# Optimization experiments

Measured on AMD Instinct MI355X. Metric: run time of the kernel, lower is better.

Reference implementation:

```python
import jax, jax.numpy as jnp
import numpy as np

N, C, T, V = 16, 64, 512, 25
R, O, S = 8, 64, 3  # rel_channels, out_channels, num_subset


def setup_inputs() -> dict:
    key = jax.random.key(0)
    ks = jax.random.split(key, 12)
    sc = 0.05
    return {
        "x": jax.random.normal(ks[0], (N, C, T, V), jnp.float32),
        "A": jax.random.normal(ks[1], (S, V, V), jnp.float32) * 0.1,
        "alpha": jax.random.normal(ks[2], (1,), jnp.float32) * 0.1,
        "w1": jax.random.normal(ks[3], (S, R, C), jnp.float32) * sc,
        "b1": jax.random.normal(ks[4], (S, R), jnp.float32) * sc,
        "w2": jax.random.normal(ks[5], (S, R, C), jnp.float32) * sc,
        "b2": jax.random.normal(ks[6], (S, R), jnp.float32) * sc,
        "w3": jax.random.normal(ks[7], (S, O, C), jnp.float32) * sc,
        "b3": jax.random.normal(ks[8], (S, O), jnp.float32) * sc,
        "w4": jax.random.normal(ks[9], (S, O, R), jnp.float32) * sc,
        "b4": jax.random.normal(ks[10], (S, O), jnp.float32) * sc,
        "sparse": 0,
    }


def _mask(w, thr):
    # SparseConv2d: magnitude-threshold the 1x1 conv weights at runtime.
    return jnp.where(jnp.abs(w) > thr, w, jnp.zeros_like(w))


def reference(x, A, alpha, w1, b1, w2, b2, w3, b3, w4, b4, sparse):
    thr = jnp.float32(sparse)

    def conv1x1(w, b, inp):  # w [o,c], b [o], inp [n,c,t,v] -> [n,o,t,v]
        return jnp.einsum('oc,nctv->notv', _mask(w, thr), inp) + b[None, :, None, None]

    y = None
    for i in range(A.shape[0]):
        x1 = conv1x1(w1[i], b1[i], x).mean(-2)          # [n,r,v]
        x2 = conv1x1(w2[i], b2[i], x).mean(-2)          # [n,r,v]
        x3 = conv1x1(w3[i], b3[i], x)                   # [n,o,t,v]
        att = jnp.tanh(x1[..., :, None] - x2[..., None, :])  # [n,r,v,v]
        a = jnp.einsum('or,nruv->nouv', _mask(w4[i], thr), att) + b4[i][None, :, None, None]
        a = a * alpha + A[i][None, None]                # [n,o,v,v]
        z = jnp.einsum('ncuv,nctu->nctv', a, x3)        # node aggregation
        y = z if y is None else y + z
    # in_channels == out_channels -> residual is identity
    return jax.nn.relu(y + x)
```

## Files before the change

kernel.cpp:

```cpp
#include <hip/hip_runtime.h>
#include <cmath>

typedef __bf16 bf16x4v __attribute__((ext_vector_type(4)));
typedef __bf16 bf16x8 __attribute__((ext_vector_type(8)));
typedef float f32x4 __attribute__((ext_vector_type(4)));

namespace {
constexpr int kN = 16, kC = 64, kT = 512, kV = 25, kS = 3, kO = 64;
constexpr int kTV = kT * kV;
constexpr size_t WS_AFRAG = 102400;
constexpr size_t WS_W3F = WS_AFRAG + (size_t)48 * 131072;
}

__device__ __forceinline__ int swzA(int col, int cbyte) {
  return ((col << 7) + cbyte) ^ ((col & 7) << 4);
}
__device__ __forceinline__ int swzB(int c, int t, int ubyte) {
  return 32768 + (c << 9) + (((t << 6) + ubyte) ^ ((((c ^ t) & 7)) << 4));
}

__global__ __launch_bounds__(256) void k1_mean(const float* __restrict__ x,
                                               float* __restrict__ xm) {
  const int bid = blockIdx.x;
  __shared__ float part[250][4];
  const int tid = threadIdx.x;
  const float4* xg4 = (const float4*)(x + (size_t)bid * kTV);
  if (tid < 250) {
    float a0 = 0.f, a1 = 0.f, a2 = 0.f, a3 = 0.f;
    for (int j = tid; j < 3200; j += 250) {
      float4 v = xg4[j];
      a0 += v.x; a1 += v.y; a2 += v.z; a3 += v.w;
    }
    part[tid][0] = a0; part[tid][1] = a1; part[tid][2] = a2; part[tid][3] = a3;
  }
  __syncthreads();
  if (tid < 25) {
    float s = 0.f;
#pragma unroll
    for (int r = 0; r < 4; ++r) {
      int q = ((tid - r + 25) % 25) * 19 % 25;
#pragma unroll
      for (int p = 0; p < 10; ++p) s += part[q + 25 * p][r];
    }
    xm[bid * 25 + tid] = s * (1.f / 512.f);
  }
}

__global__ __launch_bounds__(256) void k2_attn(
    const float* __restrict__ xm, const float* __restrict__ Ag,
    const float* __restrict__ alpha, const float* __restrict__ w1,
    const float* __restrict__ b1, const float* __restrict__ w2,
    const float* __restrict__ b2, const float* __restrict__ w3,
    const float* __restrict__ w4, const float* __restrict__ b4,
    const int* __restrict__ sparse, unsigned char* __restrict__ ws) {
  const float thr = (float)sparse[0];
  const int b = blockIdx.x;
  const int s = b >> 6, n = (b >> 2) & 15, q = b & 3;
  __shared__ float xm_l[1600];
  __shared__ float x1_l[200], x2_l[200];
  __shared__ float att_l[8 * 625];
  __shared__ float attsum_l[200];
  __shared__ float ag_l[625];
  __shared__ float acs_l[25];
  __shared__ float w4_l[512];
  const int tid = threadIdx.x;
  for (int i = tid; i < 1600; i += 256) xm_l[i] = xm[n * 1600 + i];
  for (int i = tid; i < 512; i += 256) {
    float w = w4[s * 512 + i];
    w4_l[i] = (fabsf(w) > thr) ? w : 0.f;
  }
  for (int i = tid; i < 625; i += 256) ag_l[i] = Ag[s * 625 + i];
  __syncthreads();
  for (int i = tid; i < 400; i += 256) {
    int which = i / 200, idx = i % 200, r = idx / 25, u = idx % 25;
    const float* wrow = (which == 0 ? w1 : w2) + (s * 8 + r) * 64;
    float acc = 0.f;
    for (int cc = 0; cc < 64; ++cc) {
      float w = wrow[cc];
      w = (fabsf(w) > thr) ? w : 0.f;
      acc += w * xm_l[cc * 25 + u];
    }
    acc += (which == 0 ? b1 : b2)[s * 8 + r];
    if (which == 0) x1_l[idx] = acc;
    else x2_l[idx] = acc;
  }
  __syncthreads();
  for (int i = tid; i < 8 * 625; i += 256) {
    int r = i / 625, uv = i % 625, u = uv / 25, v = uv % 25;
    att_l[i] = tanhf(x1_l[r * 25 + u] - x2_l[r * 25 + v]);
  }
  __syncthreads();
  if (tid < 200) {
    int r = tid / 25, v = tid % 25;
    float sum = 0.f;
    for (int u = 0; u < 25; ++u) sum += att_l[r * 625 + u * 25 + v];
    attsum_l[tid] = sum;
  } else if (tid < 225) {
    int v = tid - 200;
    float sum = 0.f;
    for (int u = 0; u < 25; ++u) sum += ag_l[u * 25 + v];
    acs_l[v] = sum;
  }
  __syncthreads();
  const float al = alpha[0];
  unsigned char* afrag = ws + WS_AFRAG + (size_t)(s * 16 + n) * 131072;
  for (int slot = q * 2048 + tid; slot < (q + 1) * 2048; slot += 256) {
    int c = slot >> 7, vt = (slot >> 6) & 1, l = slot & 63;
    int v = vt * 16 + (l & 15), g = l >> 4;
    bf16x8 out;
    if (v < 25) {
      float b4v = b4[s * 64 + c];
#pragma unroll
      for (int j = 0; j < 8; ++j) {
        int u = g * 8 + j;
        float val = 0.f;
        if (u < 25) {
          float acc = 0.f;
#pragma unroll
          for (int r = 0; r < 8; ++r) acc += w4_l[c * 8 + r] * att_l[r * 625 + u * 25 + v];
          val = al * (acc + b4v) + ag_l[u * 25 + v];
        } else if (u == 25) {
          float acc = 0.f;
#pragma unroll
          for (int r = 0; r < 8; ++r) acc += w4_l[c * 8 + r] * attsum_l[r * 25 + v];
          val = al * acc + 25.f * al * b4v + acs_l[v];
        }
        out[j] = (__bf16)val;
      }
    } else {
#pragma unroll
      for (int j = 0; j < 8; ++j) out[j] = (__bf16)0.f;
    }
    *(bf16x8*)(afrag + (size_t)slot * 16) = out;
  }
  if (n == 0 && tid < 128) {
    unsigned char* w3f = ws + WS_W3F + (size_t)s * 8192;
    int slot = q * 128 + tid;
    int ot = slot >> 7, ks = (slot >> 6) & 1, l = slot & 63;
    int o = ot * 16 + (l & 15), g = l >> 4;
    bf16x8 out;
#pragma unroll
    for (int j = 0; j < 8; ++j) {
      int cp = ks * 32 + g * 8 + j;
      float w = w3[(s * 64 + o) * 64 + cp];
      out[j] = (__bf16)((fabsf(w) > thr) ? w : 0.f);
    }
    *(bf16x8*)(w3f + slot * 16) = out;
  }
}

__global__ __launch_bounds__(512) void k3_main(const float* __restrict__ x,
                                               const float* __restrict__ b3,
                                               const unsigned char* __restrict__ ws,
                                               float* __restrict__ y) {
  const int n = blockIdx.x;
  const int tb = blockIdx.y;
  extern __shared__ __align__(16) unsigned char smem[];
  const int tid = threadIdx.x;
  const int w = tid >> 6, l = tid & 63, g = l >> 4, l15 = l & 15;
  const float4* xg4 = (const float4*)(x + (size_t)n * kC * kTV);

  for (int idx = tid; idx < 448; idx += 512) {
    int col_i = idx >> 3, gb = idx & 7;
    int t = col_i / 7, u = 25 + col_i % 7;
    f32x4 z = {0.f, 0.f, 0.f, 0.f};
    *(f32x4*)(smem + swzA(t * 32 + u, gb * 16)) = z;
  }
  for (int idx = tid; idx < 1536; idx += 512) {
    int pair = idx / 3, k = idx % 3;
    int c = pair >> 3, t = pair & 7;
    *(unsigned int*)(smem + swzB(c, t, 52 + 4 * k)) = 0u;
  }
  for (int i4 = tid; i4 < 3200; i4 += 512) {
    int c = i4 / 50, r4 = i4 % 50;
    float4 vv = xg4[c * 3200 + tb * 50 + r4];
    float vals[4] = {vv.x, vv.y, vv.z, vv.w};
    int lin = r4 * 4;
#pragma unroll
    for (int k = 0; k < 4; ++k) {
      int t = (lin + k) / 25, u = (lin + k) % 25;
      *(__bf16*)(smem + swzA(t * 32 + u, c * 2)) = (__bf16)vals[k];
    }
  }
  __syncthreads();

  const unsigned char* afrag = ws + WS_AFRAG;
  const unsigned char* w3f = ws + WS_W3F;

  f32x4 zacc[8][2];
#pragma unroll
  for (int cc = 0; cc < 8; ++cc)
#pragma unroll
    for (int vt = 0; vt < 2; ++vt) {
      f32x4 zz = {0.f, 0.f, 0.f, 0.f};
      zacc[cc][vt] = zz;
    }

  for (int s = 0; s < kS; ++s) {
    bf16x8 A1[4][2];
#pragma unroll
    for (int ot = 0; ot < 4; ++ot)
#pragma unroll
      for (int ks = 0; ks < 2; ++ks)
        A1[ot][ks] = *(const bf16x8*)(w3f + s * 8192 + ((ot * 2 + ks) * 64 + l) * 16);
    if (s) __syncthreads();

    f32x4 acc[2][4];
#pragma unroll
    for (int cti = 0; cti < 2; ++cti) {
      int col = w * 32 + cti * 16 + l15;
      bf16x8 xa0 = *(const bf16x8*)(smem + swzA(col, g * 16));
      bf16x8 xa1 = *(const bf16x8*)(smem + swzA(col, 64 + g * 16));
#pragma unroll
      for (int ot = 0; ot < 4; ++ot) {
        f32x4 d = {0.f, 0.f, 0.f, 0.f};
        d = __builtin_amdgcn_mfma_f32_16x16x32_bf16(xa0, A1[ot][0], d, 0, 0, 0);
        d = __builtin_amdgcn_mfma_f32_16x16x32_bf16(xa1, A1[ot][1], d, 0, 0, 0);
        acc[cti][ot] = d;
      }
    }
#pragma unroll
    for (int cti = 0; cti < 2; ++cti) {
      int u0 = cti * 16 + g * 4;
#pragma unroll
      for (int ot = 0; ot < 4; ++ot) {
        int c = ot * 16 + l15;
        if (!cti || g < 2) {
          bf16x4v pk;
          pk[0] = (__bf16)acc[cti][ot][0];
          pk[1] = (__bf16)acc[cti][ot][1];
          pk[2] = (__bf16)acc[cti][ot][2];
          pk[3] = (__bf16)acc[cti][ot][3];
          *(bf16x4v*)(smem + swzB(c, w, 2 * u0)) = pk;
        } else if (g == 2) {
          *(__bf16*)(smem + swzB(c, w, 48)) = (__bf16)acc[cti][ot][0];
        }
      }
    }
    {
      int c = tid >> 3, t = tid & 7;
      *(__bf16*)(smem + swzB(c, t, 50)) = (__bf16)b3[s * 64 + c];
    }
    const unsigned char* af = afrag + (size_t)(s * 16 + n) * 131072;
    bf16x8 b2cur0 = *(const bf16x8*)(af + ((w * 8 * 2 + 0) * 64 + l) * 16);
    bf16x8 b2cur1 = *(const bf16x8*)(af + ((w * 8 * 2 + 1) * 64 + l) * 16);
    __syncthreads();
#pragma unroll
    for (int cc = 0; cc < 8; ++cc) {
      int c = w * 8 + cc;
      bf16x8 b2n0, b2n1;
      if (cc < 7) {
        b2n0 = *(const bf16x8*)(af + (((c + 1) * 2 + 0) * 64 + l) * 16);
        b2n1 = *(const bf16x8*)(af + (((c + 1) * 2 + 1) * 64 + l) * 16);
      }
      bf16x8 a2 = *(const bf16x8*)(smem + swzB(c, l15 & 7, g * 16));
      zacc[cc][0] = __builtin_amdgcn_mfma_f32_16x16x32_bf16(a2, b2cur0, zacc[cc][0], 0, 0, 0);
      zacc[cc][1] = __builtin_amdgcn_mfma_f32_16x16x32_bf16(a2, b2cur1, zacc[cc][1], 0, 0, 0);
      if (cc < 7) {
        b2cur0 = b2n0;
        b2cur1 = b2n1;
      }
    }
  }
  __syncthreads();
  float* zs = (float*)smem;
  if (g < 2) {
#pragma unroll
    for (int cc = 0; cc < 8; ++cc) {
      int c = w * 8 + cc;
#pragma unroll
      for (int vt = 0; vt < 2; ++vt) {
        int v = vt * 16 + l15;
        if (v < 25) {
#pragma unroll
          for (int jj = 0; jj < 4; ++jj)
            zs[c * 200 + (g * 4 + jj) * 25 + v] = zacc[cc][vt][jj];
        }
      }
    }
  }
  __syncthreads();
  float4* yg4 = (float4*)(y + (size_t)n * kC * kTV);
  for (int i4 = tid; i4 < 3200; i4 += 512) {
    int c = i4 / 50, r4 = i4 % 50;
    float4 xv = xg4[c * 3200 + tb * 50 + r4];
    f32x4 zv = *(const f32x4*)(zs + c * 200 + r4 * 4);
    float4 o;
    o.x = fmaxf(zv[0] + xv.x, 0.f);
    o.y = fmaxf(zv[1] + xv.y, 0.f);
    o.z = fmaxf(zv[2] + xv.z, 0.f);
    o.w = fmaxf(zv[3] + xv.w, 0.f);
    yg4[c * 3200 + tb * 50 + r4] = o;
  }
}

extern "C" void kernel_launch(void* const* d_in, const int* in_sizes, int n_in,
                              void* d_out, int out_size, void* d_ws, size_t ws_size,
                              hipStream_t stream) {
  const float* x = (const float*)d_in[0];
  const float* Ag = (const float*)d_in[1];
  const float* alpha = (const float*)d_in[2];
  const float* w1 = (const float*)d_in[3];
  const float* b1 = (const float*)d_in[4];
  const float* w2 = (const float*)d_in[5];
  const float* b2 = (const float*)d_in[6];
  const float* w3 = (const float*)d_in[7];
  const float* b3 = (const float*)d_in[8];
  const float* w4 = (const float*)d_in[9];
  const float* b4 = (const float*)d_in[10];
  const int* sparse = (const int*)d_in[11];

  unsigned char* ws = (unsigned char*)d_ws;
  float* xm = (float*)ws;
  float* y = (float*)d_out;

  hipFuncSetAttribute((const void*)k3_main,
                      hipFuncAttributeMaxDynamicSharedMemorySize, 65536);

  k1_mean<<<kN * kC, 256, 0, stream>>>(x, xm);
  k2_attn<<<kS * kN * 4, 256, 0, stream>>>(xm, Ag, alpha, w1, b1, w2, b2, w3, w4,
                                           b4, sparse, ws);
  dim3 g3(kN, kT / 8);
  k3_main<<<g3, 512, 65536, stream>>>(x, b3, ws, y);
}
```

Measured before the change: 86.95 us.

## Load x fragments directly into registers and shrink LDS footprint in main kernel

The staged x tile in LDS is dropped: each lane now reads its bf16 MFMA A-fragment straight from global memory with scalar strided loads, so the swizzled A buffer and its zero-fill go away. The w3 weight fragments are loaded per output tile inside the loop instead of all up front, which lowers register pressure. The epilogue writes z into LDS in two channel halves, and dynamic LDS per block shrinks so more blocks can fit per CU. The cost is uncoalesced scalar global loads (stride of a full T·V plane per channel) in place of float4 loads, plus an extra barrier pair in the epilogue.

```diff
diff --git a/kernel.cpp b/kernel.cpp
--- a/kernel.cpp
+++ b/kernel.cpp
@@ -12,11 +12,8 @@
 constexpr size_t WS_W3F = WS_AFRAG + (size_t)48 * 131072;
 }
 
-__device__ __forceinline__ int swzA(int col, int cbyte) {
-  return ((col << 7) + cbyte) ^ ((col & 7) << 4);
-}
 __device__ __forceinline__ int swzB(int c, int t, int ubyte) {
-  return 32768 + (c << 9) + (((t << 6) + ubyte) ^ ((((c ^ t) & 7)) << 4));
+  return (c << 9) + (((t << 6) + ubyte) ^ ((((c ^ t) & 7)) << 4));
 }
 
 __global__ __launch_bounds__(256) void k1_mean(const float* __restrict__ x,
@@ -160,29 +157,35 @@
   const int w = tid >> 6, l = tid & 63, g = l >> 4, l15 = l & 15;
   const float4* xg4 = (const float4*)(x + (size_t)n * kC * kTV);
 
-  for (int idx = tid; idx < 448; idx += 512) {
-    int col_i = idx >> 3, gb = idx & 7;
-    int t = col_i / 7, u = 25 + col_i % 7;
-    f32x4 z = {0.f, 0.f, 0.f, 0.f};
-    *(f32x4*)(smem + swzA(t * 32 + u, gb * 16)) = z;
-  }
   for (int idx = tid; idx < 1536; idx += 512) {
     int pair = idx / 3, k = idx % 3;
     int c = pair >> 3, t = pair & 7;
     *(unsigned int*)(smem + swzB(c, t, 52 + 4 * k)) = 0u;
   }
-  for (int i4 = tid; i4 < 3200; i4 += 512) {
-    int c = i4 / 50, r4 = i4 % 50;
-    float4 vv = xg4[c * 3200 + tb * 50 + r4];
-    float vals[4] = {vv.x, vv.y, vv.z, vv.w};
-    int lin = r4 * 4;
-#pragma unroll
-    for (int k = 0; k < 4; ++k) {
-      int t = (lin + k) / 25, u = (lin + k) % 25;
-      *(__bf16*)(smem + swzA(t * 32 + u, c * 2)) = (__bf16)vals[k];
-    }
-  }
-  __syncthreads();
+
+  bf16x8 xa[2][2];
+#pragma unroll
+  for (int cti = 0; cti < 2; ++cti)
+#pragma unroll
+    for (int kf = 0; kf < 2; ++kf)
+#pragma unroll
+      for (int j = 0; j < 8; ++j) xa[cti][kf][j] = (__bf16)0.f;
+  {
+    const float* xb = x + (size_t)n * kC * kTV + (tb * 8 + w) * 25;
+#pragma unroll
+    for (int cti = 0; cti < 2; ++cti) {
+      int u = cti * 16 + l15;
+      if (u < 25) {
+#pragma unroll
+        for (int kf = 0; kf < 2; ++kf)
+#pragma unroll
+          for (int j = 0; j < 8; ++j) {
+            int cp = kf * 32 + g * 8 + j;
+            xa[cti][kf][j] = (__bf16)xb[(size_t)cp * kTV + u];
+          }
+      }
+    }
+  }
 
   const unsigned char* afrag = ws + WS_AFRAG;
   const unsigned char* w3f = ws + WS_W3F;
@@ -197,44 +200,30 @@
     }
 
   for (int s = 0; s < kS; ++s) {
-    bf16x8 A1[4][2];
-#pragma unroll
-    for (int ot = 0; ot < 4; ++ot)
-#pragma unroll
-      for (int ks = 0; ks < 2; ++ks)
-        A1[ot][ks] = *(const bf16x8*)(w3f + s * 8192 + ((ot * 2 + ks) * 64 + l) * 16);
     if (s) __syncthreads();
-
-    f32x4 acc[2][4];
-#pragma unroll
-    for (int cti = 0; cti < 2; ++cti) {
-      int col = w * 32 + cti * 16 + l15;
-      bf16x8 xa0 = *(const bf16x8*)(smem + swzA(col, g * 16));
-      bf16x8 xa1 = *(const bf16x8*)(smem + swzA(col, 64 + g * 16));
-#pragma unroll
-      for (int ot = 0; ot < 4; ++ot) {
-        f32x4 d = {0.f, 0.f, 0.f, 0.f};
-        d = __builtin_amdgcn_mfma_f32_16x16x32_bf16(xa0, A1[ot][0], d, 0, 0, 0);
-        d = __builtin_amdgcn_mfma_f32_16x16x32_bf16(xa1, A1[ot][1], d, 0, 0, 0);
-        acc[cti][ot] = d;
-      }
-    }
-#pragma unroll
-    for (int cti = 0; cti < 2; ++cti) {
-      int u0 = cti * 16 + g * 4;
-#pragma unroll
-      for (int ot = 0; ot < 4; ++ot) {
-        int c = ot * 16 + l15;
-        if (!cti || g < 2) {
-          bf16x4v pk;
-          pk[0] = (__bf16)acc[cti][ot][0];
-          pk[1] = (__bf16)acc[cti][ot][1];
-          pk[2] = (__bf16)acc[cti][ot][2];
-          pk[3] = (__bf16)acc[cti][ot][3];
-          *(bf16x4v*)(smem + swzB(c, w, 2 * u0)) = pk;
-        } else if (g == 2) {
-          *(__bf16*)(smem + swzB(c, w, 48)) = (__bf16)acc[cti][ot][0];
-        }
+#pragma unroll
+    for (int ot = 0; ot < 4; ++ot) {
+      bf16x8 wk0 = *(const bf16x8*)(w3f + s * 8192 + ((ot * 2 + 0) * 64 + l) * 16);
+      bf16x8 wk1 = *(const bf16x8*)(w3f + s * 8192 + ((ot * 2 + 1) * 64 + l) * 16);
+      f32x4 d0 = {0.f, 0.f, 0.f, 0.f}, d1 = {0.f, 0.f, 0.f, 0.f};
+      d0 = __builtin_amdgcn_mfma_f32_16x16x32_bf16(xa[0][0], wk0, d0, 0, 0, 0);
+      d0 = __builtin_amdgcn_mfma_f32_16x16x32_bf16(xa[0][1], wk1, d0, 0, 0, 0);
+      d1 = __builtin_amdgcn_mfma_f32_16x16x32_bf16(xa[1][0], wk0, d1, 0, 0, 0);
+      d1 = __builtin_amdgcn_mfma_f32_16x16x32_bf16(xa[1][1], wk1, d1, 0, 0, 0);
+      int c = ot * 16 + l15;
+      {
+        bf16x4v pk;
+        pk[0] = (__bf16)d0[0]; pk[1] = (__bf16)d0[1];
+        pk[2] = (__bf16)d0[2]; pk[3] = (__bf16)d0[3];
+        *(bf16x4v*)(smem + swzB(c, w, g * 8)) = pk;
+      }
+      if (g < 2) {
+        bf16x4v pk;
+        pk[0] = (__bf16)d1[0]; pk[1] = (__bf16)d1[1];
+        pk[2] = (__bf16)d1[2]; pk[3] = (__bf16)d1[3];
+        *(bf16x4v*)(smem + swzB(c, w, 32 + g * 8)) = pk;
+      } else if (g == 2) {
+        *(__bf16*)(smem + swzB(c, w, 48)) = (__bf16)d1[0];
       }
     }
     {
@@ -262,35 +251,37 @@
       }
     }
   }
-  __syncthreads();
-  float* zs = (float*)smem;
-  if (g < 2) {
-#pragma unroll
-    for (int cc = 0; cc < 8; ++cc) {
-      int c = w * 8 + cc;
-#pragma unroll
-      for (int vt = 0; vt < 2; ++vt) {
-        int v = vt * 16 + l15;
-        if (v < 25) {
-#pragma unroll
-          for (int jj = 0; jj < 4; ++jj)
-            zs[c * 200 + (g * 4 + jj) * 25 + v] = zacc[cc][vt][jj];
+  float* zs = (float*)(smem + 32768);
+  float4* yg4 = (float4*)(y + (size_t)n * kC * kTV);
+#pragma unroll
+  for (int h = 0; h < 2; ++h) {
+    if ((w >> 2) == h && g < 2) {
+      int c0l = (w & 3) * 8;
+#pragma unroll
+      for (int cc = 0; cc < 8; ++cc)
+#pragma unroll
+        for (int vt = 0; vt < 2; ++vt) {
+          int v = vt * 16 + l15;
+          if (v < 25) {
+#pragma unroll
+            for (int jj = 0; jj < 4; ++jj)
+              zs[(c0l + cc) * 200 + (g * 4 + jj) * 25 + v] = zacc[cc][vt][jj];
+          }
         }
-      }
-    }
-  }
-  __syncthreads();
-  float4* yg4 = (float4*)(y + (size_t)n * kC * kTV);
-  for (int i4 = tid; i4 < 3200; i4 += 512) {
-    int c = i4 / 50, r4 = i4 % 50;
-    float4 xv = xg4[c * 3200 + tb * 50 + r4];
-    f32x4 zv = *(const f32x4*)(zs + c * 200 + r4 * 4);
-    float4 o;
-    o.x = fmaxf(zv[0] + xv.x, 0.f);
-    o.y = fmaxf(zv[1] + xv.y, 0.f);
-    o.z = fmaxf(zv[2] + xv.z, 0.f);
-    o.w = fmaxf(zv[3] + xv.w, 0.f);
-    yg4[c * 3200 + tb * 50 + r4] = o;
+    }
+    __syncthreads();
+    for (int i4 = tid; i4 < 1600; i4 += 512) {
+      int cl = i4 / 50, r4 = i4 % 50, c = h * 32 + cl;
+      float4 xv = xg4[c * 3200 + tb * 50 + r4];
+      f32x4 zv = *(const f32x4*)(zs + cl * 200 + r4 * 4);
+      float4 o;
+      o.x = fmaxf(zv[0] + xv.x, 0.f);
+      o.y = fmaxf(zv[1] + xv.y, 0.f);
+      o.z = fmaxf(zv[2] + xv.z, 0.f);
+      o.w = fmaxf(zv[3] + xv.w, 0.f);
+      yg4[c * 3200 + tb * 50 + r4] = o;
+    }
+    __syncthreads();
   }
 }
 
@@ -321,5 +312,5 @@
   k2_attn<<<kS * kN * 4, 256, 0, stream>>>(xm, Ag, alpha, w1, b1, w2, b2, w3, w4,
                                            b4, sparse, ws);
   dim3 g3(kN, kT / 8);
-  k3_main<<<g3, 512, 65536, stream>>>(x, b3, ws, y);
-}
+  k3_main<<<g3, 512, 58368, stream>>>(x, b3, ws, y);
+}
```

Result: slower. 92.28 us (+6.1%).
